# Kernel tuning notes

Measured on AMD Instinct MI355X. Metric: run time of the kernel, lower is better.

The kernel has to match this reference:

```python
import jax, jax.numpy as jnp
import numpy as np

S, B, H = 2048, 2, 4096
NH, NG, HD = 32, 2, 128        # query heads, kv groups, head dim
ROT = 64                        # rotary dims (half of head dim)


def apply_rope(x, rope):
    # x: [s, b, n, hd]; rope: [s, 1, rot//2, 2]
    s = x.shape[0]
    rot = rope.shape[-2] * 2
    xr, xp = x[..., :rot], x[..., rot:]
    xs = xr.reshape(xr.shape[:-1] + (rot // 2, 2))          # [s,b,n,rot/2,2]
    rc = rope[:s].reshape(s, 1, 1, rot // 2, 2)             # broadcast over b, n
    c, sn = rc[..., 0], rc[..., 1]
    x0, x1 = xs[..., 0], xs[..., 1]
    out = jnp.stack([x0 * c - x1 * sn, x1 * c + x0 * sn], axis=-1)
    return jnp.concatenate([out.reshape(xr.shape), xp], axis=-1)


def setup_inputs() -> dict:
    key = jax.random.key(0)
    k1, k2, k3, k4 = jax.random.split(key, 4)
    hidden_states = jax.random.normal(k1, (S, B, H), dtype=jnp.float32)
    # causal boolean mask: True = attend
    causal = jnp.tril(jnp.ones((S, S), dtype=bool))
    attention_mask = jnp.broadcast_to(causal[None, None], (B, 1, S, S))
    # standard RoPE cache: [s, 1, rot//2, 2] = (cos, sin)
    pos = jnp.arange(S, dtype=jnp.float32)
    inv_freq = 1.0 / (10000.0 ** (jnp.arange(0, ROT // 2, dtype=jnp.float32) / (ROT // 2)))
    ang = pos[:, None] * inv_freq[None, :]
    rotary_pos_emb = jnp.stack([jnp.cos(ang), jnp.sin(ang)], axis=-1)[:, None]
    W_qkv = jax.random.normal(k2, (NH * HD + 2 * NG * HD, H), dtype=jnp.float32) * (H ** -0.5)
    b_qkv = jax.random.normal(k3, (NH * HD + 2 * NG * HD,), dtype=jnp.float32) * 0.02
    W_dense = jax.random.normal(k4, (H, NH * HD), dtype=jnp.float32) * ((NH * HD) ** -0.5)
    return {"hidden_states": hidden_states, "attention_mask": attention_mask,
            "rotary_pos_emb": rotary_pos_emb, "W_qkv": W_qkv, "b_qkv": b_qkv,
            "W_dense": W_dense}


def reference(hidden_states, attention_mask, rotary_pos_emb, W_qkv, b_qkv, W_dense):
    s, b, _ = hidden_states.shape
    r = NH // NG  # query heads per kv group
    mixed = jnp.einsum('sbh,oh->sbo', hidden_states, W_qkv) + b_qkv
    q = mixed[..., :NH * HD].reshape(s, b, NH, HD)
    k = mixed[..., NH * HD:NH * HD + NG * HD].reshape(s, b, NG, HD)
    v = mixed[..., NH * HD + NG * HD:].reshape(s, b, NG, HD)
    q = apply_rope(q, rotary_pos_emb)
    k = apply_rope(k, rotary_pos_emb)
    # GQA: keep kv at NG heads, give q a [g, r] split instead of materializing repeats
    qg = q.reshape(s, b, NG, r, HD)
    scale = HD ** -0.5
    scores = jnp.einsum('sbgrd,tbgd->bgrst', qg, k) * scale     # [b,g,r,s,t]
    mask = attention_mask[:, :, None]                            # [b,1,1,s,t]
    scores = jnp.where(mask, scores, jnp.finfo(scores.dtype).min)
    probs = jax.nn.softmax(scores, axis=-1)
    ctx = jnp.einsum('bgrst,tbgd->sbgrd', probs, v)              # [s,b,g,r,d]
    ctx = ctx.reshape(s, b, NH * HD)
    out = jnp.einsum('sbp,hp->sbh', ctx, W_dense)
    return out
```

## Files before the change

kernel.cpp:

```cpp
#include <hip/hip_runtime.h>
#include <cstdint>
#include <cstddef>


#define S_LEN 2048
#define BATCH 2
#define NHEADS 32
#define NGROUPS 2
#define HEADDIM 128
#define OQKV 4608
#define KSTRIDE 160
#define VSTRIDE 2080

typedef __attribute__((ext_vector_type(4))) float f32x4;
typedef __attribute__((ext_vector_type(4))) unsigned int u32x4;
typedef __attribute__((ext_vector_type(8))) unsigned short u16x8;
typedef __attribute__((ext_vector_type(8))) short s16x8;

union B8 { u32x4 q; u16x8 u; s16x8 s; };

__device__ __forceinline__ unsigned short f2b(float f) {
  unsigned int u = __builtin_bit_cast(unsigned int, f);
  u += 0x7fffu + ((u >> 16) & 1u);
  return (unsigned short)(u >> 16);
}
__device__ __forceinline__ float b2f(unsigned short h) {
  unsigned int u = ((unsigned int)h) << 16;
  return __builtin_bit_cast(float, u);
}

__device__ __forceinline__ void gload16(const unsigned short* g, unsigned short* l) {
  __builtin_amdgcn_global_load_lds(
      (const __attribute__((address_space(1))) void*)g,
      (__attribute__((address_space(3))) void*)l, 16, 0, 0);
}

__global__ __launch_bounds__(256) void cvt_kernel(const float* __restrict__ in,
                                                  unsigned short* __restrict__ out) {
  size_t i = (size_t)blockIdx.x * 256 + threadIdx.x;
  const f32x4* p = (const f32x4*)(in + i * 8);
  f32x4 a = p[0], b = p[1];
  B8 r;
  r.u[0] = f2b(a[0]); r.u[1] = f2b(a[1]); r.u[2] = f2b(a[2]); r.u[3] = f2b(a[3]);
  r.u[4] = f2b(b[0]); r.u[5] = f2b(b[1]); r.u[6] = f2b(b[2]); r.u[7] = f2b(b[3]);
  *(u32x4*)(out + i * 8) = r.q;
}

template<int HAS_BIAS, int OUT_BF16>
__global__ __launch_bounds__(512) void gemm256(const unsigned short* __restrict__ Ab,
                                               const unsigned short* __restrict__ Bt,
                                               const float* __restrict__ bias,
                                               void* __restrict__ Cp,
                                               int M, int N, int K) {
  __shared__ __align__(16) unsigned short lA[2][256 * 32];
  __shared__ __align__(16) unsigned short lB[2][256 * 32];
  const int tid = threadIdx.x;
  const int wave = tid >> 6, lane = tid & 63;
  const int quad = lane >> 4, l15 = lane & 15;
  const int wm = (wave >> 2) * 128;
  const int wn = (wave & 3) * 64;
  const int nwg = gridDim.x * gridDim.y;
  int lin = blockIdx.y * gridDim.x + blockIdx.x;
  int swz = (lin & 7) * (nwg >> 3) + (lin >> 3);
  const int bx = swz % gridDim.x, by = swz / gridDim.x;
  const int m0 = by * 256, n0 = bx * 256;
  const int sr0 = wave * 32;
  const int lrow = lane >> 2;
  const int xcol = ((lane & 3) ^ (lrow & 3)) * 8;
  const int fcol = (quad ^ (l15 & 3)) * 8;
  f32x4 acc[8][4] = {};
  const int nt = K >> 5;
  int cur = 0;

  {
    const unsigned short* Ag = Ab + (size_t)(m0 + sr0 + lrow) * K + xcol;
    const unsigned short* Bg = Bt + (size_t)(n0 + sr0 + lrow) * K + xcol;
    gload16(Ag, lA[0] + sr0 * 32);
    gload16(Ag + (size_t)16 * K, lA[0] + (sr0 + 16) * 32);
    gload16(Bg, lB[0] + sr0 * 32);
    gload16(Bg + (size_t)16 * K, lB[0] + (sr0 + 16) * 32);
  }
  __syncthreads();

  for (int t = 0; t < nt; ++t) {
    if (t + 1 < nt) {
      const int kk = (t + 1) << 5;
      const unsigned short* Ag = Ab + (size_t)(m0 + sr0 + lrow) * K + kk + xcol;
      const unsigned short* Bg = Bt + (size_t)(n0 + sr0 + lrow) * K + kk + xcol;
      unsigned short* dA = lA[cur ^ 1] + sr0 * 32;
      unsigned short* dB = lB[cur ^ 1] + sr0 * 32;
      gload16(Ag, dA);
      gload16(Ag + (size_t)16 * K, dA + 512);
      gload16(Bg, dB);
      gload16(Bg + (size_t)16 * K, dB + 512);
    }
    B8 af[8], bf[4];
#pragma unroll
    for (int i = 0; i < 8; ++i)
      af[i].q = *(const u32x4*)(lA[cur] + (wm + 16 * i + l15) * 32 + fcol);
#pragma unroll
    for (int j = 0; j < 4; ++j)
      bf[j].q = *(const u32x4*)(lB[cur] + (wn + 16 * j + l15) * 32 + fcol);
#pragma unroll
    for (int i = 0; i < 8; ++i)
#pragma unroll
      for (int j = 0; j < 4; ++j)
        acc[i][j] = __builtin_amdgcn_mfma_f32_16x16x32_bf16(af[i].s, bf[j].s, acc[i][j], 0, 0, 0);
    __syncthreads();
    cur ^= 1;
  }

#pragma unroll
  for (int i = 0; i < 8; ++i) {
    int gm = m0 + wm + 16 * i + quad * 4;
#pragma unroll
    for (int j = 0; j < 4; ++j) {
      int gn = n0 + wn + 16 * j + l15;
      float bb = HAS_BIAS ? bias[gn] : 0.0f;
#pragma unroll
      for (int r = 0; r < 4; ++r) {
        float v = acc[i][j][r] + bb;
        if (OUT_BF16)
          ((unsigned short*)Cp)[(size_t)(gm + r) * N + gn] = f2b(v);
        else
          ((float*)Cp)[(size_t)(gm + r) * N + gn] = v;
      }
    }
  }
}

__global__ __launch_bounds__(256) void rope_scatter(const unsigned short* __restrict__ mixed,
                                                    const float* __restrict__ rope,
                                                    unsigned short* __restrict__ qb,
                                                    unsigned short* __restrict__ kb,
                                                    unsigned short* __restrict__ vt) {
  unsigned int idx = blockIdx.x * 256 + threadIdx.x;
  unsigned int row = idx / 2304;
  unsigned int pr = idx - row * 2304;
  unsigned int o = pr * 2;
  unsigned int s = row >> 1, b = row & 1;
  unsigned int pq = *(const unsigned int*)(mixed + (size_t)row * OQKV + o);
  float x0 = b2f((unsigned short)(pq & 0xffff));
  float x1 = b2f((unsigned short)(pq >> 16));
  if (o >= 4352) {
    unsigned int g = (o - 4352) >> 7;
    unsigned int d = (o - 4352) & 127;
    unsigned short* base = vt + ((size_t)(b * NGROUPS + g) * HEADDIM + d) * VSTRIDE + s;
    base[0] = f2b(x0);
    base[VSTRIDE] = f2b(x1);
    return;
  }
  unsigned short* dst;
  unsigned int d;
  bool is_q = (o < 4096);
  if (is_q) {
    unsigned int h = o >> 7; d = o & 127;
    dst = qb + (((size_t)(b * NHEADS + h) * S_LEN + s) * HEADDIM + d);
  } else {
    unsigned int g = (o - 4096) >> 7; d = (o - 4096) & 127;
    dst = kb + (((size_t)(b * NGROUPS + g) * S_LEN + s) * KSTRIDE + d);
  }
  if (d < 64) {
    unsigned int i = d >> 1;
    float c = rope[s * 64 + i * 2], sn = rope[s * 64 + i * 2 + 1];
    float y0 = x0 * c - x1 * sn;
    float y1 = x1 * c + x0 * sn;
    x0 = y0; x1 = y1;
  }
  if (is_q) {
    const float scale = 0.08838834764831845f;
    x0 *= scale; x1 *= scale;
  }
  dst[0] = f2b(x0);
  dst[1] = f2b(x1);
}

__global__ __launch_bounds__(256) void attn_kernel(const unsigned short* __restrict__ qb,
                                                   const unsigned short* __restrict__ kb,
                                                   const unsigned short* __restrict__ vt,
                                                   unsigned short* __restrict__ ctx) {
  __shared__ __align__(16) unsigned short lk[64 * 128];
  __shared__ __align__(16) unsigned short lv[128 * 64];
  __shared__ __align__(16) unsigned short lp[4][16 * 72];
  const int qt = 31 - blockIdx.x;
  const int h = blockIdx.y, b = blockIdx.z;
  const int g = h >> 4;
  const int tid = threadIdx.x;
  const int wave = tid >> 6, lane = tid & 63;
  const int quad = lane >> 4, l15 = lane & 15;
  const int q0 = qt * 64 + wave * 16;
  unsigned short* lpw = lp[wave];
  char* lkb = (char*)lk;
  char* lvb = (char*)lv;

  const unsigned short* qp =
      qb + ((size_t)(b * NHEADS + h) * S_LEN + q0 + l15) * HEADDIM + quad * 8;
  B8 aq[4];
  for (int c = 0; c < 4; ++c) aq[c].q = *(const u32x4*)(qp + 32 * c);

  const unsigned short* kbase = kb + (size_t)(b * NGROUPS + g) * S_LEN * KSTRIDE;
  const unsigned short* vbase = vt + (size_t)(b * NGROUPS + g) * HEADDIM * VSTRIDE;

  const int krow = tid >> 2, kcol = (tid & 3) * 32;
  const int vrow = tid >> 1, vcol = (tid & 1) * 32;
  const int kxs = (krow & 7) << 4, vxs = (vrow & 7) << 4;
  const int kwb = krow * 256 + kcol * 2;
  const int vwb = vrow * 128 + vcol * 2;

  f32x4 o[8] = {};
  float lrow[4] = {0.f, 0.f, 0.f, 0.f};

  B8 kR0, kR1, kR2, kR3, vR0, vR1, vR2, vR3;
  {
    const unsigned short* kg = kbase + (size_t)krow * KSTRIDE + kcol;
    const unsigned short* vg = vbase + (size_t)vrow * VSTRIDE + vcol;
    kR0.q = *(const u32x4*)(kg);      kR1.q = *(const u32x4*)(kg + 8);
    kR2.q = *(const u32x4*)(kg + 16); kR3.q = *(const u32x4*)(kg + 24);
    vR0.q = *(const u32x4*)(vg);      vR1.q = *(const u32x4*)(vg + 8);
    vR2.q = *(const u32x4*)(vg + 16); vR3.q = *(const u32x4*)(vg + 24);
  }

  for (int kt = 0; kt <= qt; ++kt) {
    const int k0 = kt * 64;
    __syncthreads();
    *(u32x4*)(lkb + ((kwb +  0) ^ kxs)) = kR0.q;
    *(u32x4*)(lkb + ((kwb + 16) ^ kxs)) = kR1.q;
    *(u32x4*)(lkb + ((kwb + 32) ^ kxs)) = kR2.q;
    *(u32x4*)(lkb + ((kwb + 48) ^ kxs)) = kR3.q;
    *(u32x4*)(lvb + ((vwb +  0) ^ vxs)) = vR0.q;
    *(u32x4*)(lvb + ((vwb + 16) ^ vxs)) = vR1.q;
    *(u32x4*)(lvb + ((vwb + 32) ^ vxs)) = vR2.q;
    *(u32x4*)(lvb + ((vwb + 48) ^ vxs)) = vR3.q;
    __syncthreads();
    if (kt < qt) {
      const int k1 = k0 + 64;
      const unsigned short* kg = kbase + (size_t)(k1 + krow) * KSTRIDE + kcol;
      const unsigned short* vg = vbase + (size_t)vrow * VSTRIDE + k1 + vcol;
      kR0.q = *(const u32x4*)(kg);      kR1.q = *(const u32x4*)(kg + 8);
      kR2.q = *(const u32x4*)(kg + 16); kR3.q = *(const u32x4*)(kg + 24);
      vR0.q = *(const u32x4*)(vg);      vR1.q = *(const u32x4*)(vg + 8);
      vR2.q = *(const u32x4*)(vg + 16); vR3.q = *(const u32x4*)(vg + 24);
    }
    f32x4 sfr[4] = {};
    for (int t = 0; t < 4; ++t) {
      const int row = 16 * t + l15;
      const int rxs = (row & 7) << 4;
      const int rb = row * 256 + quad * 16;
      for (int c = 0; c < 4; ++c) {
        B8 bk;
        bk.q = *(const u32x4*)(lkb + ((rb + 64 * c) ^ rxs));
        sfr[t] = __builtin_amdgcn_mfma_f32_16x16x32_bf16(aq[c].s, bk.s, sfr[t], 0, 0, 0);
      }
    }
    const bool masked = (kt == qt);
    for (int r = 0; r < 4; ++r) {
      const int qq = q0 + quad * 4 + r;
      float psum = 0.f;
      for (int t = 0; t < 4; ++t) {
        float p = __expf(sfr[t][r]);
        if (masked && (k0 + 16 * t + l15 > qq)) p = 0.f;
        psum += p;
        lpw[(quad * 4 + r) * 72 + 16 * t + l15] = f2b(p);
      }
      lrow[r] += psum;
    }
    B8 pa0, pa1;
    pa0.q = *(const u32x4*)(lpw + l15 * 72 + quad * 8);
    pa1.q = *(const u32x4*)(lpw + l15 * 72 + 32 + quad * 8);
    for (int j = 0; j < 8; ++j) {
      const int row = 16 * j + l15;
      const int rxs = (row & 7) << 4;
      const int rb = row * 128 + quad * 16;
      B8 b0, b1;
      b0.q = *(const u32x4*)(lvb + (rb ^ rxs));
      b1.q = *(const u32x4*)(lvb + ((rb + 64) ^ rxs));
      o[j] = __builtin_amdgcn_mfma_f32_16x16x32_bf16(pa0.s, b0.s, o[j], 0, 0, 0);
      o[j] = __builtin_amdgcn_mfma_f32_16x16x32_bf16(pa1.s, b1.s, o[j], 0, 0, 0);
    }
  }
  float inv[4];
  for (int r = 0; r < 4; ++r) {
    float l = lrow[r];
    l += __shfl_xor(l, 1);
    l += __shfl_xor(l, 2);
    l += __shfl_xor(l, 4);
    l += __shfl_xor(l, 8);
    inv[r] = 1.0f / l;
  }
  for (int j = 0; j < 8; ++j) {
    for (int r = 0; r < 4; ++r) {
      int s = q0 + quad * 4 + r;
      ctx[(size_t)(s * BATCH + b) * 4096 + (size_t)h * HEADDIM + 16 * j + l15] =
          f2b(o[j][r] * inv[r]);
    }
  }
}

extern "C" void kernel_launch(void* const* d_in, const int* in_sizes, int n_in,
                              void* d_out, int out_size, void* d_ws, size_t ws_size,
                              hipStream_t stream) {
  const float* hidden = (const float*)d_in[0];
  const float* rope = (const float*)d_in[2];
  const float* Wqkv = (const float*)d_in[3];
  const float* bqkv = (const float*)d_in[4];
  const float* Wdense = (const float*)d_in[5];
  float* out = (float*)d_out;
  char* ws = (char*)d_ws;

  unsigned short* Wqkv_b   = (unsigned short*)(ws);
  unsigned short* Wdense_b = (unsigned short*)(ws + 37748736);
  unsigned short* mixedb   = (unsigned short*)(ws + 71303168);
  unsigned short* vtbuf    = (unsigned short*)(ws + 109051904);
  unsigned short* qbuf     = (unsigned short*)(ws);
  unsigned short* kbuf     = (unsigned short*)(ws + 33554432);
  unsigned short* ctxb     = (unsigned short*)(ws + 71303168);
  unsigned short* hidden_b = (unsigned short*)d_out;

  cvt_kernel<<<9216, 256, 0, stream>>>(Wqkv, Wqkv_b);
  cvt_kernel<<<8192, 256, 0, stream>>>(Wdense, Wdense_b);
  cvt_kernel<<<8192, 256, 0, stream>>>(hidden, hidden_b);

  gemm256<1, 1><<<dim3(18, 16), 512, 0, stream>>>(hidden_b, Wqkv_b, bqkv, mixedb,
                                                  4096, 4608, 4096);
  rope_scatter<<<36864, 256, 0, stream>>>(mixedb, rope, qbuf, kbuf, vtbuf);
  attn_kernel<<<dim3(32, 32, 2), 256, 0, stream>>>(qbuf, kbuf, vtbuf, ctxb);
  gemm256<0, 0><<<dim3(16, 16), 512, 0, stream>>>(ctxb, Wdense_b, nullptr, out,
                                                  4096, 4096, 4096);
}
```

Before: 964.3 us.

## Switch GEMMs to 128x128 tiles with triple-buffered LDS prefetch

```diff
diff --git a/kernel.cpp b/kernel.cpp
--- a/kernel.cpp
+++ b/kernel.cpp
@@ -47,71 +47,80 @@
 }
 
 template<int HAS_BIAS, int OUT_BF16>
-__global__ __launch_bounds__(512) void gemm256(const unsigned short* __restrict__ Ab,
+__global__ __launch_bounds__(256) void gemm128(const unsigned short* __restrict__ Ab,
                                                const unsigned short* __restrict__ Bt,
                                                const float* __restrict__ bias,
                                                void* __restrict__ Cp,
-                                               int M, int N, int K) {
-  __shared__ __align__(16) unsigned short lA[2][256 * 32];
-  __shared__ __align__(16) unsigned short lB[2][256 * 32];
+                                               int lda, int ldb, int K, int ldc) {
+  __shared__ __align__(16) unsigned short lA[3][128 * 32];
+  __shared__ __align__(16) unsigned short lB[3][128 * 32];
   const int tid = threadIdx.x;
   const int wave = tid >> 6, lane = tid & 63;
   const int quad = lane >> 4, l15 = lane & 15;
-  const int wm = (wave >> 2) * 128;
-  const int wn = (wave & 3) * 64;
+  const int wm = (wave & 1) * 64, wn = (wave >> 1) * 64;
   const int nwg = gridDim.x * gridDim.y;
   int lin = blockIdx.y * gridDim.x + blockIdx.x;
   int swz = (lin & 7) * (nwg >> 3) + (lin >> 3);
   const int bx = swz % gridDim.x, by = swz / gridDim.x;
-  const int m0 = by * 256, n0 = bx * 256;
-  const int sr0 = wave * 32;
-  const int lrow = lane >> 2;
-  const int xcol = ((lane & 3) ^ (lrow & 3)) * 8;
-  const int fcol = (quad ^ (l15 & 3)) * 8;
-  f32x4 acc[8][4] = {};
+  const int m0 = by * 128, n0 = bx * 128;
+  const int srow = wave * 32 + (lane >> 2);
+  const int scol = (lane & 3) * 8;
+  const int woff = wave * 1024;
+  f32x4 acc[4][4] = {};
   const int nt = K >> 5;
-  int cur = 0;
+  unsigned short *pA0 = lA[0], *pA1 = lA[1], *pA2 = lA[2];
+  unsigned short *pB0 = lB[0], *pB1 = lB[1], *pB2 = lB[2];
 
   {
-    const unsigned short* Ag = Ab + (size_t)(m0 + sr0 + lrow) * K + xcol;
-    const unsigned short* Bg = Bt + (size_t)(n0 + sr0 + lrow) * K + xcol;
-    gload16(Ag, lA[0] + sr0 * 32);
-    gload16(Ag + (size_t)16 * K, lA[0] + (sr0 + 16) * 32);
-    gload16(Bg, lB[0] + sr0 * 32);
-    gload16(Bg + (size_t)16 * K, lB[0] + (sr0 + 16) * 32);
-  }
-  __syncthreads();
+    const unsigned short* Ag = Ab + (size_t)(m0 + srow) * lda + scol;
+    const unsigned short* Bg = Bt + (size_t)(n0 + srow) * ldb + scol;
+    gload16(Ag, pA0 + woff);
+    gload16(Ag + (size_t)16 * lda, pA0 + woff + 512);
+    gload16(Bg, pB0 + woff);
+    gload16(Bg + (size_t)16 * ldb, pB0 + woff + 512);
+    gload16(Ag + 32, pA1 + woff);
+    gload16(Ag + (size_t)16 * lda + 32, pA1 + woff + 512);
+    gload16(Bg + 32, pB1 + woff);
+    gload16(Bg + (size_t)16 * ldb + 32, pB1 + woff + 512);
+  }
+  asm volatile("s_waitcnt vmcnt(4) lgkmcnt(0)\ns_barrier" ::: "memory");
+  __builtin_amdgcn_sched_barrier(0);
 
   for (int t = 0; t < nt; ++t) {
-    if (t + 1 < nt) {
-      const int kk = (t + 1) << 5;
-      const unsigned short* Ag = Ab + (size_t)(m0 + sr0 + lrow) * K + kk + xcol;
-      const unsigned short* Bg = Bt + (size_t)(n0 + sr0 + lrow) * K + kk + xcol;
-      unsigned short* dA = lA[cur ^ 1] + sr0 * 32;
-      unsigned short* dB = lB[cur ^ 1] + sr0 * 32;
-      gload16(Ag, dA);
-      gload16(Ag + (size_t)16 * K, dA + 512);
-      gload16(Bg, dB);
-      gload16(Bg + (size_t)16 * K, dB + 512);
-    }
-    B8 af[8], bf[4];
-#pragma unroll
-    for (int i = 0; i < 8; ++i)
-      af[i].q = *(const u32x4*)(lA[cur] + (wm + 16 * i + l15) * 32 + fcol);
+    if (t + 2 < nt) {
+      const int kk = (t + 2) << 5;
+      const unsigned short* Ag = Ab + (size_t)(m0 + srow) * lda + kk + scol;
+      const unsigned short* Bg = Bt + (size_t)(n0 + srow) * ldb + kk + scol;
+      gload16(Ag, pA2 + woff);
+      gload16(Ag + (size_t)16 * lda, pA2 + woff + 512);
+      gload16(Bg, pB2 + woff);
+      gload16(Bg + (size_t)16 * ldb, pB2 + woff + 512);
+    }
+    B8 af[4], bf[4];
+#pragma unroll
+    for (int i = 0; i < 4; ++i)
+      af[i].q = *(const u32x4*)(pA0 + (wm + 16 * i + l15) * 32 + quad * 8);
 #pragma unroll
     for (int j = 0; j < 4; ++j)
-      bf[j].q = *(const u32x4*)(lB[cur] + (wn + 16 * j + l15) * 32 + fcol);
-#pragma unroll
-    for (int i = 0; i < 8; ++i)
+      bf[j].q = *(const u32x4*)(pB0 + (wn + 16 * j + l15) * 32 + quad * 8);
+#pragma unroll
+    for (int i = 0; i < 4; ++i)
 #pragma unroll
       for (int j = 0; j < 4; ++j)
         acc[i][j] = __builtin_amdgcn_mfma_f32_16x16x32_bf16(af[i].s, bf[j].s, acc[i][j], 0, 0, 0);
-    __syncthreads();
-    cur ^= 1;
-  }
-
-#pragma unroll
-  for (int i = 0; i < 8; ++i) {
+    if (t + 1 < nt) {
+      if (t + 2 < nt)
+        asm volatile("s_waitcnt vmcnt(4) lgkmcnt(0)\ns_barrier" ::: "memory");
+      else
+        asm volatile("s_waitcnt vmcnt(0) lgkmcnt(0)\ns_barrier" ::: "memory");
+      __builtin_amdgcn_sched_barrier(0);
+      unsigned short* tA = pA0; pA0 = pA1; pA1 = pA2; pA2 = tA;
+      unsigned short* tB = pB0; pB0 = pB1; pB1 = pB2; pB2 = tB;
+    }
+  }
+
+#pragma unroll
+  for (int i = 0; i < 4; ++i) {
     int gm = m0 + wm + 16 * i + quad * 4;
 #pragma unroll
     for (int j = 0; j < 4; ++j) {
@@ -121,9 +130,9 @@
       for (int r = 0; r < 4; ++r) {
         float v = acc[i][j][r] + bb;
         if (OUT_BF16)
-          ((unsigned short*)Cp)[(size_t)(gm + r) * N + gn] = f2b(v);
+          ((unsigned short*)Cp)[(size_t)(gm + r) * ldc + gn] = f2b(v);
         else
-          ((float*)Cp)[(size_t)(gm + r) * N + gn] = v;
+          ((float*)Cp)[(size_t)(gm + r) * ldc + gn] = v;
       }
     }
   }
@@ -310,20 +319,20 @@
   unsigned short* Wqkv_b   = (unsigned short*)(ws);
   unsigned short* Wdense_b = (unsigned short*)(ws + 37748736);
   unsigned short* mixedb   = (unsigned short*)(ws + 71303168);
-  unsigned short* vtbuf    = (unsigned short*)(ws + 109051904);
   unsigned short* qbuf     = (unsigned short*)(ws);
   unsigned short* kbuf     = (unsigned short*)(ws + 33554432);
   unsigned short* ctxb     = (unsigned short*)(ws + 71303168);
   unsigned short* hidden_b = (unsigned short*)d_out;
+  unsigned short* vtbuf    = (unsigned short*)((char*)d_out + 33816576);
 
   cvt_kernel<<<9216, 256, 0, stream>>>(Wqkv, Wqkv_b);
   cvt_kernel<<<8192, 256, 0, stream>>>(Wdense, Wdense_b);
   cvt_kernel<<<8192, 256, 0, stream>>>(hidden, hidden_b);
 
-  gemm256<1, 1><<<dim3(18, 16), 512, 0, stream>>>(hidden_b, Wqkv_b, bqkv, mixedb,
-                                                  4096, 4608, 4096);
+  gemm128<1, 1><<<dim3(36, 32), 256, 0, stream>>>(hidden_b, Wqkv_b, bqkv, mixedb,
+                                                  4096, 4096, 4096, OQKV);
   rope_scatter<<<36864, 256, 0, stream>>>(mixedb, rope, qbuf, kbuf, vtbuf);
   attn_kernel<<<dim3(32, 32, 2), 256, 0, stream>>>(qbuf, kbuf, vtbuf, ctxb);
-  gemm256<0, 0><<<dim3(16, 16), 512, 0, stream>>>(ctxb, Wdense_b, nullptr, out,
-                                                  4096, 4096, 4096);
-}
+  gemm128<0, 0><<<dim3(32, 32), 256, 0, stream>>>(ctxb, Wdense_b, nullptr, out,
+                                                  4096, 4096, 4096, 4096);
+}
```

Measured after the change: 900.0 us. -6.7%, faster.
